# Performance work log

Hardware: AMD Instinct MI355X
Metric: run time of the kernel (lower is better)

## Reference

```python
import jax, jax.numpy as jnp
import numpy as np

BN_EPS = 1e-5


def setup_inputs() -> dict:
    key = jax.random.key(0)
    ks = jax.random.split(key, 5)
    B, N, M, C = 2, 8192, 8192, 3
    return {
        "x": jax.random.normal(ks[0], (B, N, C), dtype=jnp.float32),
        "y": jax.random.normal(ks[1], (B, M, C), dtype=jnp.float32),
        "W1": jax.random.normal(ks[2], (256, 20), dtype=jnp.float32) * 0.1,
        "gamma1": jnp.ones((256,), jnp.float32),
        "beta1": jnp.zeros((256,), jnp.float32),
        "mean1": jnp.zeros((256,), jnp.float32),
        "var1": jnp.ones((256,), jnp.float32),
        "W2": jax.random.normal(ks[3], (128, 256), dtype=jnp.float32) * 0.1,
        "gamma2": jnp.ones((128,), jnp.float32),
        "beta2": jnp.zeros((128,), jnp.float32),
        "mean2": jnp.zeros((128,), jnp.float32),
        "var2": jnp.ones((128,), jnp.float32),
        "W3": jax.random.normal(ks[4], (1, 128), dtype=jnp.float32) * 0.1,
        "k": 20,
    }


def _bn(x, gamma, beta, mean, var):
    # x: [B, C, N]; inference-mode BatchNorm1d
    inv = gamma * jax.lax.rsqrt(var + BN_EPS)
    return x * inv[None, :, None] + (beta - mean * inv)[None, :, None]


def reference(x, y, W1, gamma1, beta1, mean1, var1,
              W2, gamma2, beta2, mean2, var2, W3, k):
    # x: [B,N,C], y: [B,M,C]
    xx = jnp.sum(x * x, axis=-1)                      # [B,N]
    yy = jnp.sum(y * y, axis=-1)                      # [B,M]
    inner = jnp.einsum('bnc,bmc->bnm', x, y)          # [B,N,M]
    # negative squared pairwise distance (as in torch code)
    pd = 2.0 * inner - xx[:, :, None] - yy[:, None, :]
    dist, _ = jax.lax.top_k(pd, k)                    # [B,N,k], descending = k nearest
    feat = jnp.transpose(dist, (0, 2, 1))             # [B,k,N]
    h = jax.nn.relu(_bn(jnp.einsum('oc,bcn->bon', W1, feat), gamma1, beta1, mean1, var1))
    h = jax.nn.relu(_bn(jnp.einsum('oc,bcn->bon', W2, h), gamma2, beta2, mean2, var2))
    out = jax.nn.sigmoid(jnp.einsum('oc,bcn->bon', W3, h))  # [B,1,N]
    return jnp.transpose(out, (0, 2, 1))              # [B,N,1]
```

## Files before the change

kernel.cpp:

```cpp
#include <hip/hip_runtime.h>
#include <hip/hip_bf16.h>
#include <math.h>


#define M_CAND 8192
#define NROWS 16384
#define KSEL 20
#define MPL 4
#define RPW 4

typedef float v2f __attribute__((ext_vector_type(2)));

__device__ __forceinline__ float med3f(float a, float b, float c) {
    return __builtin_amdgcn_fmed3f(a, b, c);
}

__device__ __forceinline__ v2f fma2(v2f a, v2f b, v2f c) {
#if __has_builtin(__builtin_elementwise_fma)
    return __builtin_elementwise_fma(a, b, c);
#else
    v2f r; r.x = fmaf(a.x, b.x, c.x); r.y = fmaf(a.y, b.y, c.y); return r;
#endif
}

__global__ __launch_bounds__(256) void k_prep(const float* __restrict__ y,
                                              const float* __restrict__ w2,
                                              float4* __restrict__ ysp,
                                              float* __restrict__ w2t) {
    int idx = blockIdx.x * 256 + threadIdx.x;
    if (idx < 8192) {
        int b = idx >> 12, q = idx & 4095;
        const float* p0 = y + (size_t)(b * M_CAND + 2 * q) * 3;
        float a0 = p0[0], a1 = p0[1], a2 = p0[2];
        float b0 = p0[3], b1 = p0[4], b2 = p0[5];
        float nwa = -(a0 * a0 + a1 * a1 + a2 * a2);
        float nwb = -(b0 * b0 + b1 * b1 + b2 * b2);
        float4* base = ysp + b * 8192;
        base[q]        = make_float4(a0, b0, a1, b1);
        base[4096 + q] = make_float4(a2, b2, nwa, nwb);
    } else {
        int j = idx - 8192;
        int o = j >> 8, kk = j & 255;
        w2t[kk * 128 + o] = w2[j];
    }
}

__global__ __launch_bounds__(256, 4) void k_knn(const float* __restrict__ x,
                                                const float4* __restrict__ ysp,
                                                float* __restrict__ dfeat) {
    __shared__ float sm[4][64 * 21];
    const int wid  = threadIdx.x >> 6;
    const int lane = threadIdx.x & 63;
    const int qbase = (blockIdx.x * 4 + wid) * RPW;
    const int b = qbase >> 13;

    float tx0[RPW], tx1[RPW], tx2[RPW], xxn[RPW];
#pragma unroll
    for (int r = 0; r < RPW; ++r) {
        float a0 = x[(qbase + r) * 3 + 0];
        float a1 = x[(qbase + r) * 3 + 1];
        float a2 = x[(qbase + r) * 3 + 2];
        tx0[r] = 2.0f * a0; tx1[r] = 2.0f * a1; tx2[r] = 2.0f * a2;
        xxn[r] = -(a0 * a0 + a1 * a1 + a2 * a2);
    }
    const float4* pa = ysp + b * 8192 + lane;
    const float4* pb = pa + 4096;

    float bl[RPW][MPL];
#pragma unroll
    for (int r = 0; r < RPW; ++r)
#pragma unroll
        for (int j = 0; j < MPL; ++j) bl[r][j] = -3.0e38f;

#define PROCESS_PAIR(Aq, Bq)                                                   \
    {                                                                          \
        v2f y0p = {(Aq).x, (Aq).y};                                            \
        v2f y1p = {(Aq).z, (Aq).w};                                            \
        v2f y2p = {(Bq).x, (Bq).y};                                            \
        v2f nwp = {(Bq).z, (Bq).w};                                            \
        _Pragma("unroll")                                                      \
        for (int r = 0; r < RPW; ++r) {                                        \
            v2f t0 = {tx0[r], tx0[r]};                                         \
            v2f t1 = {tx1[r], tx1[r]};                                         \
            v2f t2 = {tx2[r], tx2[r]};                                         \
            v2f xp = {xxn[r], xxn[r]};                                         \
            v2f pd = fma2(t0, y0p, fma2(t1, y1p, fma2(t2, y2p, xp))) + nwp;    \
            float va = pd.x, vb = pd.y;                                        \
            bl[r][3] = med3f(va, bl[r][2], bl[r][3]);                          \
            bl[r][2] = med3f(va, bl[r][1], bl[r][2]);                          \
            bl[r][1] = med3f(va, bl[r][0], bl[r][1]);                          \
            bl[r][0] = fmaxf(bl[r][0], va);                                    \
            bl[r][3] = med3f(vb, bl[r][2], bl[r][3]);                          \
            bl[r][2] = med3f(vb, bl[r][1], bl[r][2]);                          \
            bl[r][1] = med3f(vb, bl[r][0], bl[r][1]);                          \
            bl[r][0] = fmaxf(bl[r][0], vb);                                    \
        }                                                                      \
    }

    float4 A0 = pa[0], A1 = pa[64], B0 = pb[0], B1 = pb[64];
#pragma unroll 1
    for (int t = 0; t < 32; ++t) {
        const int nt = ((t + 1) & 31) * 128;
        float4 nA0 = pa[nt], nA1 = pa[nt + 64];
        float4 nB0 = pb[nt], nB1 = pb[nt + 64];
        PROCESS_PAIR(A0, B0)
        PROCESS_PAIR(A1, B1)
        A0 = nA0; A1 = nA1; B0 = nB0; B1 = nB1;
    }

    float* myp = sm[wid] + lane * (MPL + 1);
    unsigned needmask = 0;
#pragma unroll
    for (int q = 0; q < RPW; ++q) {
#pragma unroll
        for (int j = 0; j < MPL; ++j) myp[j] = bl[q][j];
        myp[MPL] = -3.0e38f;
        asm volatile("s_waitcnt lgkmcnt(0)" ::: "memory");
        int ptr = 0;
        float sel = 0.0f;
        for (int r = 0; r < KSEL; ++r) {
            float head = myp[ptr];
            float mx = head;
#pragma unroll
            for (int off = 32; off >= 1; off >>= 1) mx = fmaxf(mx, __shfl_xor(mx, off, 64));
            unsigned long long ball = __ballot(head == mx);
            int winner = (int)__ffsll(ball) - 1;
            ptr += (lane == winner) ? 1 : 0;
            if (lane == r) sel = mx;
        }
        if (__ballot(ptr >= MPL) != 0ULL) needmask |= (1u << q);
        if (lane < KSEL) dfeat[(size_t)(qbase + q) * KSEL + lane] = sel;
    }

    if (needmask != 0) {
#pragma unroll
        for (int q = 0; q < RPW; ++q) {
            if (!(needmask & (1u << q))) continue;
            float a[KSEL];
#pragma unroll
            for (int j = 0; j < KSEL; ++j) a[j] = -3.0e38f;
#pragma unroll 1
            for (int t = 0; t < 32; ++t) {
                float4 dA0 = pa[t * 128], dA1 = pa[t * 128 + 64];
                float4 dB0 = pb[t * 128], dB1 = pb[t * 128 + 64];
                v2f t0 = {tx0[q], tx0[q]};
                v2f t1 = {tx1[q], tx1[q]};
                v2f t2 = {tx2[q], tx2[q]};
                v2f xp = {xxn[q], xxn[q]};
                v2f pd0 = fma2(t0, (v2f){dA0.x, dA0.y},
                          fma2(t1, (v2f){dA0.z, dA0.w},
                          fma2(t2, (v2f){dB0.x, dB0.y}, xp))) + (v2f){dB0.z, dB0.w};
                v2f pd1 = fma2(t0, (v2f){dA1.x, dA1.y},
                          fma2(t1, (v2f){dA1.z, dA1.w},
                          fma2(t2, (v2f){dB1.x, dB1.y}, xp))) + (v2f){dB1.z, dB1.w};
                float vv[4] = {pd0.x, pd0.y, pd1.x, pd1.y};
#pragma unroll
                for (int i = 0; i < 4; ++i) {
                    float v = vv[i];
#pragma unroll
                    for (int jj = KSEL - 1; jj >= 1; --jj) a[jj] = med3f(v, a[jj - 1], a[jj]);
                    a[0] = fmaxf(a[0], v);
                }
            }
            float* mq = sm[wid] + lane * (KSEL + 1);
#pragma unroll
            for (int j = 0; j < KSEL; ++j) mq[j] = a[j];
            mq[KSEL] = -3.0e38f;
            asm volatile("s_waitcnt lgkmcnt(0)" ::: "memory");
            int ptr2 = 0;
            float sel2 = 0.0f;
            for (int r = 0; r < KSEL; ++r) {
                float head = mq[ptr2];
                float mx = head;
#pragma unroll
                for (int off = 32; off >= 1; off >>= 1) mx = fmaxf(mx, __shfl_xor(mx, off, 64));
                unsigned long long ball = __ballot(head == mx);
                int winner = (int)__ffsll(ball) - 1;
                ptr2 += (lane == winner) ? 1 : 0;
                if (lane == r) sel2 = mx;
            }
            if (lane < KSEL) dfeat[(size_t)(qbase + q) * KSEL + lane] = sel2;
        }
    }
#undef PROCESS_PAIR
}

__global__ __launch_bounds__(256) void k_mlp(const float* __restrict__ dfeat,
                                             const float* __restrict__ W1,
                                             const float* __restrict__ g1,
                                             const float* __restrict__ be1,
                                             const float* __restrict__ mu1,
                                             const float* __restrict__ va1,
                                             const float* __restrict__ W2T,
                                             const float* __restrict__ g2,
                                             const float* __restrict__ be2,
                                             const float* __restrict__ mu2,
                                             const float* __restrict__ va2,
                                             const float* __restrict__ W3,
                                             float* __restrict__ out) {
    __shared__ float h1l[32 * 260];
    const int t = threadIdx.x;
    const int rowbase = blockIdx.x * 32;

    float w[KSEL];
#pragma unroll
    for (int j = 0; j < KSEL; j += 4) {
        float4 q = *(const float4*)(W1 + t * KSEL + j);
        w[j] = q.x; w[j + 1] = q.y; w[j + 2] = q.z; w[j + 3] = q.w;
    }
    const float s1  = g1[t] * rsqrtf(va1[t] + 1e-5f);
    const float bc1 = be1[t] - mu1[t] * s1;

    for (int r = 0; r < 32; ++r) {
        const float* dr = dfeat + (size_t)(rowbase + r) * KSEL;
        float dv[KSEL];
#pragma unroll
        for (int j = 0; j < KSEL; j += 4) {
            float4 q = *(const float4*)(dr + j);
            dv[j] = q.x; dv[j + 1] = q.y; dv[j + 2] = q.z; dv[j + 3] = q.w;
        }
        float acc0 = 0.f, acc1 = 0.f;
#pragma unroll
        for (int j = 0; j < KSEL; j += 2) {
            acc0 = fmaf(w[j], dv[j], acc0);
            acc1 = fmaf(w[j + 1], dv[j + 1], acc1);
        }
        h1l[r * 260 + t] = fmaxf(0.f, fmaf(s1, acc0 + acc1, bc1));
    }
    __syncthreads();

    const int og = t & 15;
    const int rq = t >> 4;
    float acc[2][8];
#pragma unroll
    for (int r = 0; r < 2; ++r)
#pragma unroll
        for (int i = 0; i < 8; ++i) acc[r][i] = 0.f;

    for (int kq = 0; kq < 64; ++kq) {
        const int k = kq * 4;
        float4 hq[2];
#pragma unroll
        for (int rr = 0; rr < 2; ++rr)
            hq[rr] = *(const float4*)(&h1l[(rq * 2 + rr) * 260 + k]);
        float4 wq[8];
#pragma unroll
        for (int kk = 0; kk < 4; ++kk) {
            wq[kk]     = *(const float4*)(W2T + (k + kk) * 128 + og * 4);
            wq[4 + kk] = *(const float4*)(W2T + (k + kk) * 128 + 64 + og * 4);
        }
#pragma unroll
        for (int r = 0; r < 2; ++r) {
            const float* hh = (const float*)&hq[r];
#pragma unroll
            for (int kk = 0; kk < 4; ++kk) {
                const float hval = hh[kk];
                const float* w0 = (const float*)&wq[kk];
                const float* w1 = (const float*)&wq[4 + kk];
#pragma unroll
                for (int i = 0; i < 4; ++i) {
                    acc[r][i]     = fmaf(hval, w0[i], acc[r][i]);
                    acc[r][4 + i] = fmaf(hval, w1[i], acc[r][4 + i]);
                }
            }
        }
    }

    float s2v[8], b2v[8], w3v[8];
#pragma unroll
    for (int h = 0; h < 2; ++h)
#pragma unroll
        for (int i = 0; i < 4; ++i) {
            const int o = h * 64 + og * 4 + i;
            const float sv = g2[o] * rsqrtf(va2[o] + 1e-5f);
            s2v[h * 4 + i] = sv;
            b2v[h * 4 + i] = be2[o] - mu2[o] * sv;
            w3v[h * 4 + i] = W3[o];
        }
#pragma unroll
    for (int r = 0; r < 2; ++r) {
        float c = 0.f;
#pragma unroll
        for (int i = 0; i < 8; ++i) {
            float h2 = fmaxf(0.f, fmaf(s2v[i], acc[r][i], b2v[i]));
            c = fmaf(w3v[i], h2, c);
        }
#pragma unroll
        for (int off = 8; off >= 1; off >>= 1) c += __shfl_xor(c, off, 64);
        if (og == 0) {
            float z = c;
            out[rowbase + rq * 2 + r] = 1.0f / (1.0f + expf(-z));
        }
    }
}

extern "C" void kernel_launch(void* const* d_in, const int* in_sizes, int n_in,
                              void* d_out, int out_size, void* d_ws, size_t ws_size,
                              hipStream_t stream) {
    const float* x   = (const float*)d_in[0];
    const float* y   = (const float*)d_in[1];
    const float* W1  = (const float*)d_in[2];
    const float* g1  = (const float*)d_in[3];
    const float* be1 = (const float*)d_in[4];
    const float* mu1 = (const float*)d_in[5];
    const float* va1 = (const float*)d_in[6];
    const float* W2  = (const float*)d_in[7];
    const float* g2  = (const float*)d_in[8];
    const float* be2 = (const float*)d_in[9];
    const float* mu2 = (const float*)d_in[10];
    const float* va2 = (const float*)d_in[11];
    const float* W3  = (const float*)d_in[12];
    float* out = (float*)d_out;

    char* ws = (char*)d_ws;
    float4* ysp  = (float4*)(ws);
    float* dfeat = (float*)(ws + 262144);
    float* w2t   = (float*)(ws + 262144 + 1310720);

    k_prep<<<160, 256, 0, stream>>>(y, W2, ysp, w2t);
    k_knn <<<1024, 256, 0, stream>>>(x, ysp, dfeat);
    k_mlp <<<512, 256, 0, stream>>>(dfeat, W1, g1, be1, mu1, va1,
                                    w2t, g2, be2, mu2, va2, W3, out);
}
```

Before: 128.1 us.

## Stage candidate tiles in shared memory and merge per-lane lists in registers

The kNN kernel now loads candidate points cooperatively into shared-memory tiles of 256 pairs, double-buffered through registers, so all four waves of a block share each tile instead of each wave reading global/L2 separately. The per-lane sorted candidate lists are merged across lanes with register shifts instead of LDS staging and indexed loads. The tiling adds two block barriers per tile, which may stall waves. The register-based pop also drops LDS traffic but adds select instructions per round.

New measurement: 127.0 us. About the same (-0.9%).

```diff
diff --git a/kernel.cpp b/kernel.cpp
--- a/kernel.cpp
+++ b/kernel.cpp
@@ -8,6 +8,8 @@
 #define KSEL 20
 #define MPL 4
 #define RPW 4
+#define TPAIRS 256
+#define NTILES 16
 
 typedef float v2f __attribute__((ext_vector_type(2)));
 
@@ -48,9 +50,11 @@
 __global__ __launch_bounds__(256, 4) void k_knn(const float* __restrict__ x,
                                                 const float4* __restrict__ ysp,
                                                 float* __restrict__ dfeat) {
-    __shared__ float sm[4][64 * 21];
-    const int wid  = threadIdx.x >> 6;
-    const int lane = threadIdx.x & 63;
+    __shared__ float4 tileA[TPAIRS];
+    __shared__ float4 tileB[TPAIRS];
+    const int tid  = threadIdx.x;
+    const int wid  = tid >> 6;
+    const int lane = tid & 63;
     const int qbase = (blockIdx.x * 4 + wid) * RPW;
     const int b = qbase >> 13;
 
@@ -63,8 +67,8 @@
         tx0[r] = 2.0f * a0; tx1[r] = 2.0f * a1; tx2[r] = 2.0f * a2;
         xxn[r] = -(a0 * a0 + a1 * a1 + a2 * a2);
     }
-    const float4* pa = ysp + b * 8192 + lane;
-    const float4* pb = pa + 4096;
+    const float4* ybA = ysp + b * 8192;
+    const float4* ybB = ybA + 4096;
 
     float bl[RPW][MPL];
 #pragma unroll
@@ -97,38 +101,48 @@
         }                                                                      \
     }
 
-    float4 A0 = pa[0], A1 = pa[64], B0 = pb[0], B1 = pb[64];
+    float4 rA = ybA[tid], rB = ybB[tid];
 #pragma unroll 1
-    for (int t = 0; t < 32; ++t) {
-        const int nt = ((t + 1) & 31) * 128;
-        float4 nA0 = pa[nt], nA1 = pa[nt + 64];
-        float4 nB0 = pb[nt], nB1 = pb[nt + 64];
-        PROCESS_PAIR(A0, B0)
-        PROCESS_PAIR(A1, B1)
-        A0 = nA0; A1 = nA1; B0 = nB0; B1 = nB1;
-    }
-
-    float* myp = sm[wid] + lane * (MPL + 1);
+    for (int t = 0; t < NTILES; ++t) {
+        tileA[tid] = rA;
+        tileB[tid] = rB;
+        __syncthreads();
+        if (t + 1 < NTILES) {
+            rA = ybA[(t + 1) * TPAIRS + tid];
+            rB = ybB[(t + 1) * TPAIRS + tid];
+        }
+        const float4* tA = tileA + lane;
+        const float4* tB = tileB + lane;
+#pragma unroll
+        for (int j = 0; j < 4; ++j) {
+            float4 A = tA[j * 64];
+            float4 Bv = tB[j * 64];
+            PROCESS_PAIR(A, Bv)
+        }
+        __syncthreads();
+    }
+
     unsigned needmask = 0;
 #pragma unroll
     for (int q = 0; q < RPW; ++q) {
-#pragma unroll
-        for (int j = 0; j < MPL; ++j) myp[j] = bl[q][j];
-        myp[MPL] = -3.0e38f;
-        asm volatile("s_waitcnt lgkmcnt(0)" ::: "memory");
-        int ptr = 0;
+        float h0 = bl[q][0], h1 = bl[q][1], h2 = bl[q][2], h3 = bl[q][3];
+        int pops = 0;
         float sel = 0.0f;
         for (int r = 0; r < KSEL; ++r) {
-            float head = myp[ptr];
-            float mx = head;
+            float mx = h0;
 #pragma unroll
             for (int off = 32; off >= 1; off >>= 1) mx = fmaxf(mx, __shfl_xor(mx, off, 64));
-            unsigned long long ball = __ballot(head == mx);
+            unsigned long long ball = __ballot(h0 == mx);
             int winner = (int)__ffsll(ball) - 1;
-            ptr += (lane == winner) ? 1 : 0;
+            bool win = (lane == winner);
+            h0 = win ? h1 : h0;
+            h1 = win ? h2 : h1;
+            h2 = win ? h3 : h2;
+            h3 = win ? -3.0e38f : h3;
+            pops += win ? 1 : 0;
             if (lane == r) sel = mx;
         }
-        if (__ballot(ptr >= MPL) != 0ULL) needmask |= (1u << q);
+        if (__ballot(pops >= MPL) != 0ULL) needmask |= (1u << q);
         if (lane < KSEL) dfeat[(size_t)(qbase + q) * KSEL + lane] = sel;
     }
 
@@ -141,8 +155,8 @@
             for (int j = 0; j < KSEL; ++j) a[j] = -3.0e38f;
 #pragma unroll 1
             for (int t = 0; t < 32; ++t) {
-                float4 dA0 = pa[t * 128], dA1 = pa[t * 128 + 64];
-                float4 dB0 = pb[t * 128], dB1 = pb[t * 128 + 64];
+                float4 dA0 = ybA[t * 128 + lane], dA1 = ybA[t * 128 + 64 + lane];
+                float4 dB0 = ybB[t * 128 + lane], dB1 = ybB[t * 128 + 64 + lane];
                 v2f t0 = {tx0[q], tx0[q]};
                 v2f t1 = {tx1[q], tx1[q]};
                 v2f t2 = {tx2[q], tx2[q]};
@@ -162,21 +176,17 @@
                     a[0] = fmaxf(a[0], v);
                 }
             }
-            float* mq = sm[wid] + lane * (KSEL + 1);
-#pragma unroll
-            for (int j = 0; j < KSEL; ++j) mq[j] = a[j];
-            mq[KSEL] = -3.0e38f;
-            asm volatile("s_waitcnt lgkmcnt(0)" ::: "memory");
-            int ptr2 = 0;
             float sel2 = 0.0f;
             for (int r = 0; r < KSEL; ++r) {
-                float head = mq[ptr2];
-                float mx = head;
+                float mx = a[0];
 #pragma unroll
                 for (int off = 32; off >= 1; off >>= 1) mx = fmaxf(mx, __shfl_xor(mx, off, 64));
-                unsigned long long ball = __ballot(head == mx);
+                unsigned long long ball = __ballot(a[0] == mx);
                 int winner = (int)__ffsll(ball) - 1;
-                ptr2 += (lane == winner) ? 1 : 0;
+                bool win = (lane == winner);
+#pragma unroll
+                for (int jj = 0; jj < KSEL - 1; ++jj) a[jj] = win ? a[jj + 1] : a[jj];
+                a[KSEL - 1] = win ? -3.0e38f : a[KSEL - 1];
                 if (lane == r) sel2 = mx;
             }
             if (lane < KSEL) dfeat[(size_t)(qbase + q) * KSEL + lane] = sel2;
@@ -288,8 +298,7 @@
 #pragma unroll
         for (int off = 8; off >= 1; off >>= 1) c += __shfl_xor(c, off, 64);
         if (og == 0) {
-            float z = c;
-            out[rowbase + rq * 2 + r] = 1.0f / (1.0f + expf(-z));
+            out[rowbase + rq * 2 + r] = 1.0f / (1.0f + expf(-c));
         }
     }
 }
```
